# Kernel tuning notes

Measured on AMD Instinct MI355X. Metric: run time of the kernel, lower is better.

Reference implementation:

```python
import jax, jax.numpy as jnp
import numpy as np

EPS = 1e-12  # matches torch F.normalize default eps


def _l2_normalize(x, axis):
    n = jnp.sqrt(jnp.sum(x * x, axis=axis, keepdims=True))
    return x / jnp.maximum(n, EPS)


def setup_inputs() -> dict:
    key = jax.random.key(0)
    k1, k2, k3, k4 = jax.random.split(key, 4)
    B, Din, T = 8, 1024, 2048
    Dcb, V = 64, 8192
    z = jax.random.normal(k1, (B, Din, T), dtype=jnp.float32)
    W = jax.random.normal(k2, (Dcb, Din), dtype=jnp.float32) * 0.02
    b = jax.random.normal(k3, (Dcb,), dtype=jnp.float32) * 0.02
    codebook = jax.random.normal(k4, (V, Dcb), dtype=jnp.float32)
    return {"z": z, "W": W, "b": b, "codebook": codebook}


def reference(z, W, b, codebook):
    # in_project: 1x1 Conv1d over channels -> per-timestep linear
    # z: [B, Din, T], W: [Dcb, Din] -> z_e: [B, Dcb, T]
    z_e = jnp.einsum('bct,dc->bdt', z, W) + b[None, :, None]
    B, Dcb, T = z_e.shape
    encodings = z_e.transpose(0, 2, 1).reshape(B * T, Dcb)  # [N, Dcb]
    en = _l2_normalize(encodings, axis=1)
    cn = _l2_normalize(codebook, axis=1)
    # squared L2 distance between unit vectors (kept in the original expanded form)
    dist = (jnp.sum(en * en, axis=1, keepdims=True)
            - 2.0 * (en @ cn.T)
            + jnp.sum(cn * cn, axis=1)[None, :])  # [N, V]
    indices = jnp.argmax(-dist, axis=1).reshape(B, T)
    return indices
```

## Files before the change

kernel.cpp:

```cpp
#include <hip/hip_runtime.h>
#include <math.h>

#define BB    8
#define DIN   1024
#define TT    2048
#define DCB   64
#define VV    8192
#define NN    (BB * TT)
#define EPSN  1e-12f

#define DSPLIT 4
#define CPCHUNK (VV / DSPLIT)
#define TCODES 32
#define TSTEPS  (CPCHUNK / TCODES)

typedef float f32x4  __attribute__((ext_vector_type(4)));
typedef float f32x16 __attribute__((ext_vector_type(16)));
typedef int   i32x16 __attribute__((ext_vector_type(16)));
typedef _Float16 half8 __attribute__((ext_vector_type(8)));

typedef const __attribute__((address_space(1))) void* gas_ptr;
typedef __attribute__((address_space(3))) void* las_ptr;

__global__ void __launch_bounds__(256) k_prep_cb(const float* __restrict__ cb,
                                                 _Float16* __restrict__ ch,
                                                 _Float16* __restrict__ cl,
                                                 float* __restrict__ c2) {
    int v    = blockIdx.x * 4 + (threadIdx.x >> 6);
    int k    = threadIdx.x & 63;
    float x  = cb[v * DCB + k];
    float s  = x * x;
    #pragma unroll
    for (int off = 32; off; off >>= 1) s += __shfl_xor(s, off, 64);
    float den = fmaxf(sqrtf(s), EPSN);
    float c   = x / den;

    _Float16 h = (_Float16)c;
    float r    = c - (float)h;
    ch[v * DCB + k] = h;
    cl[v * DCB + k] = (_Float16)(r * 2048.0f);

    float s2 = c * c;
    #pragma unroll
    for (int off = 32; off; off >>= 1) s2 += __shfl_xor(s2, off, 64);
    if (k == 0) c2[v] = s2;
}

__global__ void __launch_bounds__(256) k_prep_wt(const float* __restrict__ W,
                                                 float* __restrict__ wt) {
    int i = blockIdx.x * 256 + threadIdx.x;
    int d = i >> 10;
    int c = i & 1023;
    wt[c * DCB + d] = W[d * DIN + c];
}

__global__ void __launch_bounds__(256, 2)
k_gemm_part(const float* __restrict__ z, const float* __restrict__ wt,
            float* __restrict__ part, int kch) {
    __shared__ __align__(1024) float wlds[256 * 64];

    int tid  = threadIdx.x;
    int lane = tid & 63;
    int wv   = tid >> 6;
    int d0   = wv * 16;
    int n0   = blockIdx.x * 256;
    int ks   = blockIdx.y;
    int c0   = ks * kch;
    int b    = n0 >> 11;
    int t0   = (n0 & 2047) + lane * 4;

    {
        const f32x4* wsrc = (const f32x4*)(wt + (size_t)c0 * DCB);
        int ncalls = kch / 16;
        for (int k = 0; k < ncalls; ++k) {
            int ub = k * 256 + wv * 64;
            __builtin_amdgcn_global_load_lds((gas_ptr)(wsrc + ub + lane),
                                             (las_ptr)((f32x4*)wlds + ub), 16, 0, 0);
        }
    }
    asm volatile("s_waitcnt vmcnt(0)" ::: "memory");
    __syncthreads();

    const float* zp = z + (size_t)b * (DIN * TT) + (size_t)c0 * TT + t0;

    f32x4 acc[4][4];
    #pragma unroll
    for (int i = 0; i < 4; ++i)
        #pragma unroll
        for (int j = 0; j < 4; ++j) acc[i][j] = (f32x4)0.0f;

    #pragma unroll 8
    for (int c = 0; c < kch; ++c) {
        f32x4 zv = *(const f32x4*)(zp + (size_t)c * TT);
        const f32x4* wr = (const f32x4*)&wlds[c * DCB + d0];
        f32x4 w0 = wr[0], w1 = wr[1], w2 = wr[2], w3 = wr[3];
        #pragma unroll
        for (int tq = 0; tq < 4; ++tq) {
            float zs = zv[tq];
            acc[tq][0] += w0 * zs;
            acc[tq][1] += w1 * zs;
            acc[tq][2] += w2 * zs;
            acc[tq][3] += w3 * zs;
        }
    }

    float* pp = part + ((size_t)ks * NN + n0 + lane * 4) * DCB + d0;
    #pragma unroll
    for (int tq = 0; tq < 4; ++tq) {
        f32x4* dst = (f32x4*)(pp + (size_t)tq * DCB);
        dst[0] = acc[tq][0];
        dst[1] = acc[tq][1];
        dst[2] = acc[tq][2];
        dst[3] = acc[tq][3];
    }
}

__global__ void __launch_bounds__(256) k_combine(const float* __restrict__ part,
                                                 const float* __restrict__ bias,
                                                 _Float16* __restrict__ eh,
                                                 _Float16* __restrict__ el,
                                                 int ksplit) {
    int gid = blockIdx.x * 256 + threadIdx.x;
    int n   = gid >> 3;
    int d0  = (gid & 7) * 8;

    float ze[8];
    #pragma unroll
    for (int j = 0; j < 8; ++j) ze[j] = bias[d0 + j];

    for (int ks = 0; ks < ksplit; ++ks) {
        const float4* pp = (const float4*)(part + ((size_t)ks * NN + n) * DCB + d0);
        float4 p0 = pp[0], p1 = pp[1];
        ze[0] += p0.x; ze[1] += p0.y; ze[2] += p0.z; ze[3] += p0.w;
        ze[4] += p1.x; ze[5] += p1.y; ze[6] += p1.z; ze[7] += p1.w;
    }

    float ss = 0.0f;
    #pragma unroll
    for (int j = 0; j < 8; ++j) ss = fmaf(ze[j], ze[j], ss);
    ss += __shfl_xor(ss, 1, 64);
    ss += __shfl_xor(ss, 2, 64);
    ss += __shfl_xor(ss, 4, 64);
    float den = fmaxf(sqrtf(ss), EPSN);

    half8 vh, vl;
    #pragma unroll
    for (int j = 0; j < 8; ++j) {
        float x = ze[j] / den;
        _Float16 h = (_Float16)x;
        vh[j] = h;
        vl[j] = (_Float16)((x - (float)h) * 2048.0f);
    }
    *(half8*)&eh[(size_t)n * DCB + d0] = vh;
    *(half8*)&el[(size_t)n * DCB + d0] = vl;
}

__global__ void __launch_bounds__(256) k_distmax(const _Float16* __restrict__ eh,
                                                 const _Float16* __restrict__ el,
                                                 const _Float16* __restrict__ chg,
                                                 const _Float16* __restrict__ clg,
                                                 const float* __restrict__ c2,
                                                 float* __restrict__ pscore,
                                                 int* __restrict__ pidx) {
    __shared__ __align__(1024) char smem[2][2][4096];

    int tid  = threadIdx.x;
    int w    = tid >> 6;
    int lane = tid & 63;
    int rr   = lane & 31;
    int hhf  = lane >> 5;
    int chunk = blockIdx.y;
    int v0   = chunk * CPCHUNK;
    int m0   = blockIdx.x * 128 + w * 32;

    const char* ehp = (const char*)(eh + (size_t)(m0 + rr) * DCB) + hhf * 16;
    const char* elp = (const char*)(el + (size_t)(m0 + rr) * DCB) + hhf * 16;
    half8 ah0 = *(const half8*)(ehp +  0), ah1 = *(const half8*)(ehp + 32);
    half8 ah2 = *(const half8*)(ehp + 64), ah3 = *(const half8*)(ehp + 96);
    half8 al0 = *(const half8*)(elp +  0), al1 = *(const half8*)(elp + 32);
    half8 al2 = *(const half8*)(elp + 64), al3 = *(const half8*)(elp + 96);
    asm volatile("" : "+v"(ah0), "+v"(ah1), "+v"(ah2), "+v"(ah3),
                      "+v"(al0), "+v"(al1), "+v"(al2), "+v"(al3));

    #define STAGE(b, t)                                                          \
    {                                                                            \
        const char* chs = (const char*)chg + ((size_t)(v0 + (t) * 32)) * 128;    \
        const char* cls = (const char*)clg + ((size_t)(v0 + (t) * 32)) * 128;    \
        _Pragma("unroll")                                                        \
        for (int j = 0; j < 2; ++j) {                                            \
            int cc   = w * 2 + j;                                                \
            int prt  = cc & 3;                                                   \
            int lin  = prt * 1024 + (lane << 4);                                 \
            int so   = lin ^ (((lin >> 7) & 7) << 4);                            \
            const char* gs = (cc < 4 ? chs : cls) + so;                          \
            __builtin_amdgcn_global_load_lds((gas_ptr)gs,                        \
                (las_ptr)&smem[b][cc >= 4][prt * 1024], 16, 0, 0);               \
        }                                                                        \
    }

    STAGE(0, 0);

    f32x16 kz;
    f32x16 best;
    i32x16 bidx;
    #pragma unroll
    for (int i = 0; i < 16; ++i) { kz[i] = 0.0f; best[i] = -INFINITY; bidx[i] = 0; }

    asm volatile("s_waitcnt vmcnt(0)" ::: "memory");
    __syncthreads();

    int lin0 = rr * 128 + hhf * 16;

    for (int t = 0; t < TSTEPS; ++t) {
        int cur = t & 1;
        if (t + 1 < TSTEPS) STAGE(cur ^ 1, t + 1);

        int   vcode = v0 + t * 32 + rr;
        float c2v   = c2[vcode];

        #define SWZ(x) ((x) ^ ((((x) >> 7) & 7) << 4))
        half8 bh0 = *(const half8*)&smem[cur][0][SWZ(lin0 +  0)];
        half8 bh1 = *(const half8*)&smem[cur][0][SWZ(lin0 + 32)];
        half8 bh2 = *(const half8*)&smem[cur][0][SWZ(lin0 + 64)];
        half8 bh3 = *(const half8*)&smem[cur][0][SWZ(lin0 + 96)];
        half8 bl0 = *(const half8*)&smem[cur][1][SWZ(lin0 +  0)];
        half8 bl1 = *(const half8*)&smem[cur][1][SWZ(lin0 + 32)];
        half8 bl2 = *(const half8*)&smem[cur][1][SWZ(lin0 + 64)];
        half8 bl3 = *(const half8*)&smem[cur][1][SWZ(lin0 + 96)];
        #undef SWZ

        f32x16 Ahh, Amid;
        Ahh  = __builtin_amdgcn_mfma_f32_32x32x16_f16(ah0, bh0, kz, 0, 0, 0);
        Amid = __builtin_amdgcn_mfma_f32_32x32x16_f16(ah0, bl0, kz, 0, 0, 0);
        Amid = __builtin_amdgcn_mfma_f32_32x32x16_f16(al0, bh0, Amid, 0, 0, 0);
        Ahh  = __builtin_amdgcn_mfma_f32_32x32x16_f16(ah1, bh1, Ahh, 0, 0, 0);
        Amid = __builtin_amdgcn_mfma_f32_32x32x16_f16(ah1, bl1, Amid, 0, 0, 0);
        Amid = __builtin_amdgcn_mfma_f32_32x32x16_f16(al1, bh1, Amid, 0, 0, 0);
        Ahh  = __builtin_amdgcn_mfma_f32_32x32x16_f16(ah2, bh2, Ahh, 0, 0, 0);
        Amid = __builtin_amdgcn_mfma_f32_32x32x16_f16(ah2, bl2, Amid, 0, 0, 0);
        Amid = __builtin_amdgcn_mfma_f32_32x32x16_f16(al2, bh2, Amid, 0, 0, 0);
        Ahh  = __builtin_amdgcn_mfma_f32_32x32x16_f16(ah3, bh3, Ahh, 0, 0, 0);
        Amid = __builtin_amdgcn_mfma_f32_32x32x16_f16(ah3, bl3, Amid, 0, 0, 0);
        Amid = __builtin_amdgcn_mfma_f32_32x32x16_f16(al3, bh3, Amid, 0, 0, 0);

        #pragma unroll
        for (int i = 0; i < 16; ++i) {
            float dot = fmaf(Amid[i], 4.8828125e-4f, Ahh[i]);
            float s   = fmaf(2.0f, dot, -c2v);
            bool  g   = s > best[i];
            best[i]   = g ? s : best[i];
            bidx[i]   = g ? vcode : bidx[i];
        }

        asm volatile("s_waitcnt vmcnt(0)" ::: "memory");
        __syncthreads();
    }
    #undef STAGE

    #pragma unroll
    for (int i = 0; i < 16; ++i) {
        float bv = best[i];
        int   bi = bidx[i];
        #pragma unroll
        for (int off = 1; off < 32; off <<= 1) {
            float ob = __shfl_xor(bv, off, 64);
            int   oi = __shfl_xor(bi, off, 64);
            if (ob > bv || (ob == bv && oi < bi)) { bv = ob; bi = oi; }
        }
        if (rr == 0) {
            int row = m0 + (i & 3) + 8 * (i >> 2) + 4 * hhf;
            pscore[(size_t)chunk * NN + row] = bv;
            pidx  [(size_t)chunk * NN + row] = bi;
        }
    }
}

__global__ void __launch_bounds__(256) k_reduce(const float* __restrict__ pscore,
                                                const int* __restrict__ pidx,
                                                int* __restrict__ out) {
    int n = blockIdx.x * 256 + threadIdx.x;
    float best = -INFINITY;
    int   bi   = 0;
    #pragma unroll
    for (int c = 0; c < DSPLIT; ++c) {
        float s = pscore[(size_t)c * NN + n];
        int  id = pidx [(size_t)c * NN + n];
        if (s > best) { best = s; bi = id; }
    }
    out[n] = bi;
}

extern "C" void kernel_launch(void* const* d_in, const int* in_sizes, int n_in,
                              void* d_out, int out_size, void* d_ws, size_t ws_size,
                              hipStream_t stream) {
    const float* z  = (const float*)d_in[0];
    const float* W  = (const float*)d_in[1];
    const float* bi = (const float*)d_in[2];
    const float* cb = (const float*)d_in[3];
    int* out = (int*)d_out;

    char* ws = (char*)d_ws;
    _Float16* ch  = (_Float16*)(ws);
    _Float16* cl  = (_Float16*)(ws + 1048576);
    float*    c2  = (float*)   (ws + 2097152);
    float*    wt  = (float*)   (ws + 2129920);
    _Float16* eh  = (_Float16*)(ws + 2392064);
    _Float16* el  = (_Float16*)(ws + 4489216);
    float* pscore = (float*)   (ws + 6586368);
    int*   pidx   = (int*)     (ws + 6848512);
    float* part   = (float*)   (ws + 7110656);

    const size_t need8 = 7110656ULL + (size_t)8 * NN * DCB * 4;
    int ksplit = (ws_size >= need8) ? 8 : 4;
    int kch    = DIN / ksplit;

    hipLaunchKernelGGL(k_prep_cb,   dim3(VV / 4),          dim3(256), 0, stream, cb, ch, cl, c2);
    hipLaunchKernelGGL(k_prep_wt,   dim3(DIN * DCB / 256), dim3(256), 0, stream, W, wt);
    hipLaunchKernelGGL(k_gemm_part, dim3(NN / 256, ksplit), dim3(256), 0, stream, z, wt, part, kch);
    hipLaunchKernelGGL(k_combine,   dim3(NN * 8 / 256),    dim3(256), 0, stream, part, bi, eh, el, ksplit);
    hipLaunchKernelGGL(k_distmax,   dim3(NN / 128, DSPLIT), dim3(256), 0, stream,
                       eh, el, ch, cl, c2, pscore, pidx);
    hipLaunchKernelGGL(k_reduce,    dim3(NN / 256),        dim3(256), 0, stream, pscore, pidx, out);
}
```

Before: 121.7 us.

## Give each wave private double-buffered codebook LDS tiles and drop block barriers

Each of the four waves now stages the full 32-code codebook tile (hi and lo halves) into its own private double-buffered LDS region, so the per-step __syncthreads is removed and only a per-wave vmcnt wait remains. The prefetch of the next tile is issued after the current tile's LDS reads. This removes block-wide barrier stalls between waves. In exchange the kernel does four times the global-to-LDS codebook traffic and its LDS footprint grows to 64 KB per block, which can cut the number of blocks resident per CU.

```diff
diff --git a/kernel.cpp b/kernel.cpp
--- a/kernel.cpp
+++ b/kernel.cpp
@@ -162,7 +162,7 @@
                                                  const float* __restrict__ c2,
                                                  float* __restrict__ pscore,
                                                  int* __restrict__ pidx) {
-    __shared__ __align__(1024) char smem[2][2][4096];
+    __shared__ __align__(1024) char smem[4][2][2][4096];
 
     int tid  = threadIdx.x;
     int w    = tid >> 6;
@@ -187,14 +187,13 @@
         const char* chs = (const char*)chg + ((size_t)(v0 + (t) * 32)) * 128;    \
         const char* cls = (const char*)clg + ((size_t)(v0 + (t) * 32)) * 128;    \
         _Pragma("unroll")                                                        \
-        for (int j = 0; j < 2; ++j) {                                            \
-            int cc   = w * 2 + j;                                                \
-            int prt  = cc & 3;                                                   \
+        for (int j = 0; j < 8; ++j) {                                            \
+            int prt  = j & 3;                                                    \
             int lin  = prt * 1024 + (lane << 4);                                 \
             int so   = lin ^ (((lin >> 7) & 7) << 4);                            \
-            const char* gs = (cc < 4 ? chs : cls) + so;                          \
+            const char* gs = (j < 4 ? chs : cls) + so;                           \
             __builtin_amdgcn_global_load_lds((gas_ptr)gs,                        \
-                (las_ptr)&smem[b][cc >= 4][prt * 1024], 16, 0, 0);               \
+                (las_ptr)&smem[w][b][j >= 4][prt * 1024], 16, 0, 0);             \
         }                                                                        \
     }
 
@@ -206,28 +205,30 @@
     #pragma unroll
     for (int i = 0; i < 16; ++i) { kz[i] = 0.0f; best[i] = -INFINITY; bidx[i] = 0; }
 
-    asm volatile("s_waitcnt vmcnt(0)" ::: "memory");
-    __syncthreads();
-
     int lin0 = rr * 128 + hhf * 16;
 
     for (int t = 0; t < TSTEPS; ++t) {
         int cur = t & 1;
-        if (t + 1 < TSTEPS) STAGE(cur ^ 1, t + 1);
+
+        asm volatile("s_waitcnt vmcnt(0)" ::: "memory");
 
         int   vcode = v0 + t * 32 + rr;
         float c2v   = c2[vcode];
 
         #define SWZ(x) ((x) ^ ((((x) >> 7) & 7) << 4))
-        half8 bh0 = *(const half8*)&smem[cur][0][SWZ(lin0 +  0)];
-        half8 bh1 = *(const half8*)&smem[cur][0][SWZ(lin0 + 32)];
-        half8 bh2 = *(const half8*)&smem[cur][0][SWZ(lin0 + 64)];
-        half8 bh3 = *(const half8*)&smem[cur][0][SWZ(lin0 + 96)];
-        half8 bl0 = *(const half8*)&smem[cur][1][SWZ(lin0 +  0)];
-        half8 bl1 = *(const half8*)&smem[cur][1][SWZ(lin0 + 32)];
-        half8 bl2 = *(const half8*)&smem[cur][1][SWZ(lin0 + 64)];
-        half8 bl3 = *(const half8*)&smem[cur][1][SWZ(lin0 + 96)];
+        const char* sh = &smem[w][cur][0][0];
+        const char* sl = &smem[w][cur][1][0];
+        half8 bh0 = *(const half8*)(sh + SWZ(lin0 +  0));
+        half8 bh1 = *(const half8*)(sh + SWZ(lin0 + 32));
+        half8 bh2 = *(const half8*)(sh + SWZ(lin0 + 64));
+        half8 bh3 = *(const half8*)(sh + SWZ(lin0 + 96));
+        half8 bl0 = *(const half8*)(sl + SWZ(lin0 +  0));
+        half8 bl1 = *(const half8*)(sl + SWZ(lin0 + 32));
+        half8 bl2 = *(const half8*)(sl + SWZ(lin0 + 64));
+        half8 bl3 = *(const half8*)(sl + SWZ(lin0 + 96));
         #undef SWZ
+
+        if (t + 1 < TSTEPS) STAGE(cur ^ 1, t + 1);
 
         f32x16 Ahh, Amid;
         Ahh  = __builtin_amdgcn_mfma_f32_32x32x16_f16(ah0, bh0, kz, 0, 0, 0);
@@ -251,9 +252,6 @@
             best[i]   = g ? s : best[i];
             bidx[i]   = g ? vcode : bidx[i];
         }
-
-        asm volatile("s_waitcnt vmcnt(0)" ::: "memory");
-        __syncthreads();
     }
     #undef STAGE
 
```

Result: slower. 131.4 us (+8.0%).
